# Kernel optimization log

Measured on AMD Instinct MI355X. Metric: run time of the kernel, lower is better.

The kernel has to match this reference:

```python
import jax, jax.numpy as jnp
jax.config.update("jax_enable_x64", True)  # original computes in float64
import numpy as np

ALPHA = 0.01  # init kwarg


def setup_inputs() -> dict:
    key = jax.random.key(0)
    x = jax.random.normal(key, (8, 8192, 512), dtype=jnp.float32)
    return {"x": x}


def reference(x):
    # x: [B, T, C]
    _, t, _ = x.shape
    # powers = flip(arange(t)) = [t-1, t-2, ..., 0]
    powers = jnp.arange(t - 1, -1, -1, dtype=jnp.float64)
    base = jnp.power(1.0 - ALPHA, powers)          # (1-alpha)^(t-1-i), [T]
    divisor = base.reshape(1, t, 1)                # [1, T, 1]
    weights = base.at[1:].multiply(ALPHA).reshape(1, t, 1)
    out = jnp.cumsum(x.astype(jnp.float64) * weights, axis=1) / divisor
    return out.astype(x.dtype)
```

## Files before the change

### kernel.cpp

```cpp
#include <hip/hip_runtime.h>
#include <math.h>


namespace {
constexpr int B = 8;
constexpr int T = 8192;
constexpr int C = 512;
constexpr float ALPHA = 0.01f;
constexpr float DECAY = 1.0f - ALPHA;
constexpr int S4 = C / 4;
constexpr int TPB = S4;

typedef float f32x4 __attribute__((ext_vector_type(4)));

__device__ __forceinline__ void ema_step(float4& y, const float4 v) {
    y.x = DECAY * y.x + ALPHA * v.x;
    y.y = DECAY * y.y + ALPHA * v.y;
    y.z = DECAY * y.z + ALPHA * v.z;
    y.w = DECAY * y.w + ALPHA * v.w;
}
}

template <int CHUNK>
__global__ __launch_bounds__(TPB) void ema_ends(const float* __restrict__ x,
                                                float* __restrict__ ends) {
    constexpr int K = T / CHUNK;
    const int k = blockIdx.x;
    const int b = blockIdx.y;
    const int tid = threadIdx.x;
    const float4* xp = reinterpret_cast<const float4*>(x) +
                       (size_t)(b * T + k * CHUNK) * S4 + tid;
    float4 y;
    if (k == 0) {
        y = xp[0];
    } else {
        y = make_float4(0.f, 0.f, 0.f, 0.f);
    }
#pragma unroll 8
    for (int t = 0; t < CHUNK; ++t) {
        float4 v = xp[(size_t)t * S4];
        ema_step(y, v);
    }
    reinterpret_cast<float4*>(ends)[(size_t)(b * K + k) * S4 + tid] = y;
}

template <int CHUNK>
__global__ __launch_bounds__(TPB) void ema_carry(float* ends, float dC) {
    constexpr int K = T / CHUNK;
    const int b = blockIdx.x;
    const int tid = threadIdx.x;
    float4* ep = reinterpret_cast<float4*>(ends) + (size_t)b * K * S4 + tid;
    float4 y = ep[0];
#pragma unroll 8
    for (int m = 1; m < K; ++m) {
        float4 e = ep[(size_t)m * S4];
        ep[(size_t)m * S4] = y;
        y.x = dC * y.x + e.x;
        y.y = dC * y.y + e.y;
        y.z = dC * y.z + e.z;
        y.w = dC * y.w + e.w;
    }
}

template <int CHUNK>
__global__ __launch_bounds__(TPB) void ema_apply(const float* __restrict__ x,
                                                 const float* __restrict__ carry,
                                                 float* __restrict__ out) {
    constexpr int K = T / CHUNK;
    const int k = blockIdx.x;
    const int b = blockIdx.y;
    const int tid = threadIdx.x;
    const size_t base4 = (size_t)(b * T + k * CHUNK) * S4 + tid;
    const float4* xp = reinterpret_cast<const float4*>(x) + base4;
    float4* op = reinterpret_cast<float4*>(out) + base4;

    float4 y;
    if (k == 0) {
        y = xp[0];
    } else {
        y = reinterpret_cast<const float4*>(carry)[(size_t)(b * K + k) * S4 + tid];
    }
#pragma unroll 8
    for (int t = 0; t < CHUNK; ++t) {
        float4 v = xp[(size_t)t * S4];
        ema_step(y, v);
        __builtin_nontemporal_store(*reinterpret_cast<const f32x4*>(&y),
                                    reinterpret_cast<f32x4*>(op + (size_t)t * S4));
    }
}

__global__ __launch_bounds__(TPB) void ema_seq_kernel(const float* __restrict__ x,
                                                      float* __restrict__ out) {
    const int b = blockIdx.x;
    const int tid = threadIdx.x;
    const float4* xp = reinterpret_cast<const float4*>(x) + (size_t)b * T * S4 + tid;
    float4* op = reinterpret_cast<float4*>(out) + (size_t)b * T * S4 + tid;
    float4 y = xp[0];
    for (int t = 0; t < T; ++t) {
        float4 v = xp[(size_t)t * S4];
        ema_step(y, v);
        op[(size_t)t * S4] = y;
    }
}

extern "C" void kernel_launch(void* const* d_in, const int* in_sizes, int n_in,
                              void* d_out, int out_size, void* d_ws, size_t ws_size,
                              hipStream_t stream) {
    (void)in_sizes; (void)n_in; (void)out_size;
    const float* x = reinterpret_cast<const float*>(d_in[0]);
    float* out = reinterpret_cast<float*>(d_out);

    constexpr int CH = 32;
    constexpr int KCH = T / CH;
    const size_t need = (size_t)B * KCH * C * sizeof(float);

    constexpr int CH2 = 128;
    constexpr int KCH2 = T / CH2;
    const size_t need2 = (size_t)B * KCH2 * C * sizeof(float);

    if (ws_size >= need) {
        float* ends = reinterpret_cast<float*>(d_ws);
        const float dC = (float)pow((double)DECAY, (double)CH);
        ema_ends<CH><<<dim3(KCH, B), dim3(TPB), 0, stream>>>(x, ends);
        ema_carry<CH><<<dim3(B), dim3(TPB), 0, stream>>>(ends, dC);
        ema_apply<CH><<<dim3(KCH, B), dim3(TPB), 0, stream>>>(x, ends, out);
    } else if (ws_size >= need2) {
        float* ends = reinterpret_cast<float*>(d_ws);
        const float dC = (float)pow((double)DECAY, (double)CH2);
        ema_ends<CH2><<<dim3(KCH2, B), dim3(TPB), 0, stream>>>(x, ends);
        ema_carry<CH2><<<dim3(B), dim3(TPB), 0, stream>>>(ends, dC);
        ema_apply<CH2><<<dim3(KCH2, B), dim3(TPB), 0, stream>>>(x, ends, out);
    } else {
        ema_seq_kernel<<<dim3(B), dim3(TPB), 0, stream>>>(x, out);
    }
}
```

Measured before the change: 272.4 us.

## Replace serial carry kernel with truncated windowed fold inside apply kernel

```diff
diff --git a/kernel.cpp b/kernel.cpp
--- a/kernel.cpp
+++ b/kernel.cpp
@@ -10,6 +10,9 @@
 constexpr float DECAY = 1.0f - ALPHA;
 constexpr int S4 = C / 4;
 constexpr int TPB = S4;
+constexpr int CHUNK = 64;
+constexpr int K = T / CHUNK;
+constexpr int W = 32;
 
 typedef float f32x4 __attribute__((ext_vector_type(4)));
 
@@ -21,10 +24,8 @@
 }
 }
 
-template <int CHUNK>
 __global__ __launch_bounds__(TPB) void ema_ends(const float* __restrict__ x,
                                                 float* __restrict__ ends) {
-    constexpr int K = T / CHUNK;
     const int k = blockIdx.x;
     const int b = blockIdx.y;
     const int tid = threadIdx.x;
@@ -44,29 +45,10 @@
     reinterpret_cast<float4*>(ends)[(size_t)(b * K + k) * S4 + tid] = y;
 }
 
-template <int CHUNK>
-__global__ __launch_bounds__(TPB) void ema_carry(float* ends, float dC) {
-    constexpr int K = T / CHUNK;
-    const int b = blockIdx.x;
-    const int tid = threadIdx.x;
-    float4* ep = reinterpret_cast<float4*>(ends) + (size_t)b * K * S4 + tid;
-    float4 y = ep[0];
-#pragma unroll 8
-    for (int m = 1; m < K; ++m) {
-        float4 e = ep[(size_t)m * S4];
-        ep[(size_t)m * S4] = y;
-        y.x = dC * y.x + e.x;
-        y.y = dC * y.y + e.y;
-        y.z = dC * y.z + e.z;
-        y.w = dC * y.w + e.w;
-    }
-}
-
-template <int CHUNK>
-__global__ __launch_bounds__(TPB) void ema_apply(const float* __restrict__ x,
-                                                 const float* __restrict__ carry,
-                                                 float* __restrict__ out) {
-    constexpr int K = T / CHUNK;
+__global__ __launch_bounds__(TPB) void ema_fold_apply(const float* __restrict__ x,
+                                                      const float* __restrict__ ends,
+                                                      float* __restrict__ out,
+                                                      float dC) {
     const int k = blockIdx.x;
     const int b = blockIdx.y;
     const int tid = threadIdx.x;
@@ -78,7 +60,19 @@
     if (k == 0) {
         y = xp[0];
     } else {
-        y = reinterpret_cast<const float4*>(carry)[(size_t)(b * K + k) * S4 + tid];
+        y = make_float4(0.f, 0.f, 0.f, 0.f);
+        const float4* ep = reinterpret_cast<const float4*>(ends) +
+                           (size_t)b * K * S4 + tid;
+        int m0 = k - W;
+        if (m0 < 0) m0 = 0;
+#pragma unroll 8
+        for (int m = m0; m < k; ++m) {
+            float4 e = ep[(size_t)m * S4];
+            y.x = dC * y.x + e.x;
+            y.y = dC * y.y + e.y;
+            y.z = dC * y.z + e.z;
+            y.w = dC * y.w + e.w;
+        }
     }
 #pragma unroll 8
     for (int t = 0; t < CHUNK; ++t) {
@@ -110,26 +104,12 @@
     const float* x = reinterpret_cast<const float*>(d_in[0]);
     float* out = reinterpret_cast<float*>(d_out);
 
-    constexpr int CH = 32;
-    constexpr int KCH = T / CH;
-    const size_t need = (size_t)B * KCH * C * sizeof(float);
-
-    constexpr int CH2 = 128;
-    constexpr int KCH2 = T / CH2;
-    const size_t need2 = (size_t)B * KCH2 * C * sizeof(float);
-
+    const size_t need = (size_t)B * K * C * sizeof(float);
     if (ws_size >= need) {
         float* ends = reinterpret_cast<float*>(d_ws);
-        const float dC = (float)pow((double)DECAY, (double)CH);
-        ema_ends<CH><<<dim3(KCH, B), dim3(TPB), 0, stream>>>(x, ends);
-        ema_carry<CH><<<dim3(B), dim3(TPB), 0, stream>>>(ends, dC);
-        ema_apply<CH><<<dim3(KCH, B), dim3(TPB), 0, stream>>>(x, ends, out);
-    } else if (ws_size >= need2) {
-        float* ends = reinterpret_cast<float*>(d_ws);
-        const float dC = (float)pow((double)DECAY, (double)CH2);
-        ema_ends<CH2><<<dim3(KCH2, B), dim3(TPB), 0, stream>>>(x, ends);
-        ema_carry<CH2><<<dim3(B), dim3(TPB), 0, stream>>>(ends, dC);
-        ema_apply<CH2><<<dim3(KCH2, B), dim3(TPB), 0, stream>>>(x, ends, out);
+        const float dC = (float)pow((double)DECAY, (double)CHUNK);
+        ema_ends<<<dim3(K, B), dim3(TPB), 0, stream>>>(x, ends);
+        ema_fold_apply<<<dim3(K, B), dim3(TPB), 0, stream>>>(x, ends, out, dC);
     } else {
         ema_seq_kernel<<<dim3(B), dim3(TPB), 0, stream>>>(x, out);
     }
```

After: 250.8 us, median of 2. 7.9% less time.
